# Optimization experiments

Measured on AMD Instinct MI355X. Metric: run time of the kernel, lower is better.

The kernel has to match this reference:

```python
import jax, jax.numpy as jnp
import numpy as np

# --- static configuration (mirrors init_kwargs) ---
L = 16        # latent_size
HL = 512      # hypernet_layer_size
D = 64        # decoder_layer_size
NDEC = 2      # decoder_n_layers
B, G = 128, 100  # batch, grid (pressure levels)
LOGP_MEAN, LOGP_STD = 0.0, 3.0
T_MEAN, T_STD = 1500.0, 500.0

# decoder layer structure generated by the hypernet
WEIGHT_SIZES = [(1, D)] + [(D, D)] * NDEC + [(D, 1)]
BIAS_SIZES = [1] + [D] * NDEC + [1]
OUT_SIZE = sum(a * b for a, b in WEIGHT_SIZES) + sum(BIAS_SIZES)  # 8450


def setup_inputs() -> dict:
    key = jax.random.key(0)
    ks = jax.random.split(key, 8)
    def init(k, shape, fan_in):
        return (jax.random.normal(k, shape, jnp.float32) / np.float32(np.sqrt(fan_in)))
    return {
        "z": jax.random.normal(ks[0], (B, L), jnp.float32),
        "log_P": jax.random.normal(ks[1], (B, G), jnp.float32) * 2.0,
        # hypernet MLP params: L -> HL -> HL -> HL -> OUT_SIZE
        "hW0": init(ks[2], (L, HL), L), "hb0": jnp.zeros((HL,), jnp.float32),
        "hW1": init(ks[3], (HL, HL), HL), "hb1": jnp.zeros((HL,), jnp.float32),
        "hW2": init(ks[4], (HL, HL), HL), "hb2": jnp.zeros((HL,), jnp.float32),
        "hWo": init(ks[5], (HL, OUT_SIZE), HL), "hbo": jnp.zeros((OUT_SIZE,), jnp.float32),
    }


def reference(z, log_P, hW0, hb0, hW1, hb1, hW2, hb2, hWo, hbo):
    Bsz, Gsz = log_P.shape
    R = Bsz * Gsz  # flattened rows
    # broadcast latent over the pressure grid: (B, L) -> (R, L)
    z_flat = jnp.broadcast_to(z[:, None, :], (Bsz, Gsz, z.shape[-1])).reshape(R, -1)
    # normalize pressure -> decoder input, shape (R, 1)
    x = (log_P.reshape(R, 1) - LOGP_MEAN) / LOGP_STD
    # hypernet MLP (leaky_relu, slope 0.01 like torch default)
    h = jax.nn.leaky_relu(z_flat @ hW0 + hb0)
    h = jax.nn.leaky_relu(h @ hW1 + hb1)
    h = jax.nn.leaky_relu(h @ hW2 + hb2)
    wab = h @ hWo + hbo  # (R, OUT_SIZE): per-row decoder weights+biases
    # per-row decoder: chain of batched GEMVs with siren activation
    off = 0
    n_layers = len(WEIGHT_SIZES)
    for i, ((di, do), bs) in enumerate(zip(WEIGHT_SIZES, BIAS_SIZES)):
        n = di * do
        w = wab[:, off:off + n].reshape(R, di, do)
        b = wab[:, off + n:off + n + bs]  # broadcasts against (R, do)
        off += n + bs
        x = jnp.einsum('bi,bij->bj', x, w) + b
        if i == 0:
            x = x * 30.0  # siren first-layer omega_0
        if i < n_layers - 1:
            x = jnp.sin(x)  # siren activation; last layer is Identity
    T_pred = x.reshape(Bsz, Gsz)
    # undo temperature normalization
    return T_pred * T_STD + T_MEAN
```

## Files before the change

### kernel.cpp

```cpp
#include <hip/hip_runtime.h>

#define WSTRIDE 8704

__device__ __forceinline__ float lrelu(float x) { return x > 0.0f ? x : 0.01f * x; }

__global__ __launch_bounds__(128) void h0T_kernel(const float* __restrict__ z,
                                                  const float* __restrict__ W,
                                                  const float* __restrict__ bias,
                                                  float* __restrict__ h0T) {
    int j = blockIdx.x;
    int b = threadIdx.x;
    float zr[16];
    *(float4*)&zr[0]  = *(const float4*)&z[b * 16 + 0];
    *(float4*)&zr[4]  = *(const float4*)&z[b * 16 + 4];
    *(float4*)&zr[8]  = *(const float4*)&z[b * 16 + 8];
    *(float4*)&zr[12] = *(const float4*)&z[b * 16 + 12];
    float acc = bias[j];
#pragma unroll
    for (int l = 0; l < 16; ++l) acc = fmaf(zr[l], W[l * 512 + j], acc);
    h0T[j * 128 + b] = lrelu(acc);
}

__global__ __launch_bounds__(512) void gemmT_kernel(const float* __restrict__ At,
                                                    const float* __restrict__ W,
                                                    const float* __restrict__ bias,
                                                    float* __restrict__ OT) {
    __shared__ __align__(16) float As[512][4];
    __shared__ float red[8][64][5];
    int jt = blockIdx.x & 7;
    int bt = blockIdx.x >> 3;
    int tid = threadIdx.x;
    int lane = tid & 63;
    int wid  = __builtin_amdgcn_readfirstlane(tid >> 6);
    int b0 = bt * 4;
#pragma unroll
    for (int r = 0; r < 2; ++r) {
        int p = r * 512 + tid;
        int k = p >> 1, q = p & 1;
        *(float2*)&As[k][q * 2] = *(const float2*)&At[k * 128 + b0 + q * 2];
    }
    __syncthreads();
    int j = jt * 64 + lane;
    float acc[4] = {};
    int k0 = wid * 64;
#pragma unroll 8
    for (int kk = 0; kk < 64; ++kk) {
        int k = k0 + kk;
        float4 a = *(const float4*)&As[k][0];
        float w = W[k * 512 + j];
        acc[0] = fmaf(a.x, w, acc[0]);
        acc[1] = fmaf(a.y, w, acc[1]);
        acc[2] = fmaf(a.z, w, acc[2]);
        acc[3] = fmaf(a.w, w, acc[3]);
    }
#pragma unroll
    for (int i = 0; i < 4; ++i) red[wid][lane][i] = acc[i];
    __syncthreads();
    if (tid < 256) {
        int jj = tid >> 2;
        int bb = tid & 3;
        float s = 0.f;
#pragma unroll
        for (int w = 0; w < 8; ++w) s += red[w][jj][bb];
        int jg = jt * 64 + jj;
        OT[jg * 128 + b0 + bb] = lrelu(s + bias[jg]);
    }
}

__global__ __launch_bounds__(256) void wabT_kernel(const float* __restrict__ At,
                                                   const float* __restrict__ W,
                                                   const float* __restrict__ bias,
                                                   float* __restrict__ wab) {
    __shared__ __align__(16) float smem[4352];
    float (*As)[8] = (float (*)[8])smem;
    int tid = threadIdx.x;
    int lane = tid & 63;
    int wid = __builtin_amdgcn_readfirstlane(tid >> 6);
    int jt = blockIdx.x >> 4;
    int bt = blockIdx.x & 15;
    if (jt >= 67) return;
    int b0 = bt * 8;
#pragma unroll
    for (int r = 0; r < 8; ++r) {
        int p = r * 256 + tid;
        int k = p >> 1, h = (p & 1) * 4;
        *(float4*)&As[k][h] = *(const float4*)&At[k * 128 + b0 + h];
    }
    __syncthreads();
    int j0r = jt * 128 + lane * 2;
    int j0 = j0r <= 8448 ? j0r : 8448;
    int k0 = wid * 128;
    const float* __restrict__ Wp = W + (size_t)k0 * 8450 + j0;
    float acc[8][2];
#pragma unroll
    for (int i = 0; i < 8; ++i) { acc[i][0] = 0.f; acc[i][1] = 0.f; }
#pragma unroll 4
    for (int kk = 0; kk < 128; ++kk) {
        float4 aL = *(const float4*)&As[k0 + kk][0];
        float4 aH = *(const float4*)&As[k0 + kk][4];
        float2 w = *(const float2*)(Wp + (size_t)kk * 8450);
        float av[8] = {aL.x, aL.y, aL.z, aL.w, aH.x, aH.y, aH.z, aH.w};
#pragma unroll
        for (int i = 0; i < 8; ++i) {
            acc[i][0] = fmaf(av[i], w.x, acc[i][0]);
            acc[i][1] = fmaf(av[i], w.y, acc[i][1]);
        }
    }
    __syncthreads();
#pragma unroll
    for (int i = 0; i < 8; ++i) {
        smem[(wid * 8 + i) * 132 + lane * 2 + 0] = acc[i][0];
        smem[(wid * 8 + i) * 132 + lane * 2 + 1] = acc[i][1];
    }
    __syncthreads();
    int j = tid & 127;
    int bs = tid >> 7;
    int jg = jt * 128 + j;
    if (jg < 8450) {
        float bj = bias[jg];
        int dst = jg + (jg >= 65 ? 3 : 0);
#pragma unroll
        for (int q = 0; q < 4; ++q) {
            int bb = bs * 4 + q;
            float s = smem[(0 * 8 + bb) * 132 + j] + smem[(1 * 8 + bb) * 132 + j]
                    + smem[(2 * 8 + bb) * 132 + j] + smem[(3 * 8 + bb) * 132 + j];
            wab[(size_t)(b0 + bb) * WSTRIDE + dst] = s + bj;
        }
    }
}

__global__ __launch_bounds__(512) void decoder_kernel(const float* __restrict__ wab,
                                                      const float* __restrict__ logP,
                                                      float* __restrict__ out) {
    __shared__ float hX[64 * 65];
    __shared__ float hY[64 * 65];
    __shared__ float red[8][68];
    int b  = blockIdx.x >> 1;
    int gh = blockIdx.x & 1;
    int tid = threadIdx.x;
    int lane = tid & 63;
    int jq = (tid >> 6) * 8;
    int g = gh * 64 + lane;
    bool act = g < 100;
    const float* __restrict__ row = wab + (size_t)b * WSTRIDE;
    float x0 = act ? logP[b * 100 + g] * (1.0f / 3.0f) : 0.0f;
    float c0 = row[64];
#pragma unroll
    for (int t = 0; t < 8; ++t)
        hX[(jq + t) * 65 + lane] = __sinf(30.0f * fmaf(x0, row[jq + t], c0));
    __syncthreads();
    {
        float a[8];
#pragma unroll
        for (int t = 0; t < 8; ++t) a[t] = row[4164 + jq + t];
#pragma unroll 4
        for (int i = 0; i < 64; ++i) {
            float hi = hX[i * 65 + lane];
            const float* wr = row + 68 + i * 64 + jq;
            float4 w0 = *(const float4*)&wr[0];
            float4 w1 = *(const float4*)&wr[4];
            a[0] = fmaf(hi, w0.x, a[0]);  a[1] = fmaf(hi, w0.y, a[1]);
            a[2] = fmaf(hi, w0.z, a[2]);  a[3] = fmaf(hi, w0.w, a[3]);
            a[4] = fmaf(hi, w1.x, a[4]);  a[5] = fmaf(hi, w1.y, a[5]);
            a[6] = fmaf(hi, w1.z, a[6]);  a[7] = fmaf(hi, w1.w, a[7]);
        }
#pragma unroll
        for (int t = 0; t < 8; ++t) hY[(jq + t) * 65 + lane] = __sinf(a[t]);
    }
    __syncthreads();
    {
        float a[8];
#pragma unroll
        for (int t = 0; t < 8; ++t) a[t] = row[8324 + jq + t];
#pragma unroll 4
        for (int i = 0; i < 64; ++i) {
            float hi = hY[i * 65 + lane];
            const float* wr = row + 4228 + i * 64 + jq;
            float4 w0 = *(const float4*)&wr[0];
            float4 w1 = *(const float4*)&wr[4];
            a[0] = fmaf(hi, w0.x, a[0]);  a[1] = fmaf(hi, w0.y, a[1]);
            a[2] = fmaf(hi, w0.z, a[2]);  a[3] = fmaf(hi, w0.w, a[3]);
            a[4] = fmaf(hi, w1.x, a[4]);  a[5] = fmaf(hi, w1.y, a[5]);
            a[6] = fmaf(hi, w1.z, a[6]);  a[7] = fmaf(hi, w1.w, a[7]);
        }
#pragma unroll
        for (int t = 0; t < 8; ++t) hX[(jq + t) * 65 + lane] = __sinf(a[t]);
    }
    __syncthreads();
    float p = 0.f;
#pragma unroll
    for (int t = 0; t < 8; ++t)
        p = fmaf(hX[(jq + t) * 65 + lane], row[8388 + jq + t], p);
    red[tid >> 6][lane] = p;
    __syncthreads();
    if (tid < 64 && act) {
        float s = row[8452];
#pragma unroll
        for (int w = 0; w < 8; ++w) s += red[w][lane];
        out[b * 100 + g] = fmaf(s, 500.0f, 1500.0f);
    }
}

extern "C" void kernel_launch(void* const* d_in, const int* in_sizes, int n_in,
                              void* d_out, int out_size, void* d_ws, size_t ws_size,
                              hipStream_t stream) {
    const float* z    = (const float*)d_in[0];
    const float* logP = (const float*)d_in[1];
    const float* hW0  = (const float*)d_in[2];
    const float* hb0  = (const float*)d_in[3];
    const float* hW1  = (const float*)d_in[4];
    const float* hb1  = (const float*)d_in[5];
    const float* hW2  = (const float*)d_in[6];
    const float* hb2  = (const float*)d_in[7];
    const float* hWo  = (const float*)d_in[8];
    const float* hbo  = (const float*)d_in[9];
    float* out = (float*)d_out;

    float* wab = (float*)d_ws;
    float* h0T = wab + 128 * WSTRIDE;
    float* h1T = h0T + 512 * 128;
    float* h2T = h1T + 512 * 128;

    h0T_kernel<<<512, 128, 0, stream>>>(z, hW0, hb0, h0T);
    gemmT_kernel<<<256, 512, 0, stream>>>(h0T, hW1, hb1, h1T);
    gemmT_kernel<<<256, 512, 0, stream>>>(h1T, hW2, hb2, h2T);
    wabT_kernel<<<1088, 256, 0, stream>>>(h2T, hWo, hbo, wab);
    decoder_kernel<<<256, 512, 0, stream>>>(wab, logP, out);
}
```

Baseline: 69.18 us.

## Fuse all five stages into one cooperative persistent kernel with grid syncs

```diff
diff --git a/kernel.cpp b/kernel.cpp
--- a/kernel.cpp
+++ b/kernel.cpp
@@ -1,35 +1,21 @@
 #include <hip/hip_runtime.h>
+#include <hip/hip_cooperative_groups.h>
+
+namespace cg = cooperative_groups;
 
 #define WSTRIDE 8704
 
 __device__ __forceinline__ float lrelu(float x) { return x > 0.0f ? x : 0.01f * x; }
 
-__global__ __launch_bounds__(128) void h0T_kernel(const float* __restrict__ z,
-                                                  const float* __restrict__ W,
-                                                  const float* __restrict__ bias,
-                                                  float* __restrict__ h0T) {
-    int j = blockIdx.x;
-    int b = threadIdx.x;
-    float zr[16];
-    *(float4*)&zr[0]  = *(const float4*)&z[b * 16 + 0];
-    *(float4*)&zr[4]  = *(const float4*)&z[b * 16 + 4];
-    *(float4*)&zr[8]  = *(const float4*)&z[b * 16 + 8];
-    *(float4*)&zr[12] = *(const float4*)&z[b * 16 + 12];
-    float acc = bias[j];
-#pragma unroll
-    for (int l = 0; l < 16; ++l) acc = fmaf(zr[l], W[l * 512 + j], acc);
-    h0T[j * 128 + b] = lrelu(acc);
-}
-
-__global__ __launch_bounds__(512) void gemmT_kernel(const float* __restrict__ At,
-                                                    const float* __restrict__ W,
-                                                    const float* __restrict__ bias,
-                                                    float* __restrict__ OT) {
-    __shared__ __align__(16) float As[512][4];
-    __shared__ float red[8][64][5];
+__device__ __forceinline__ void gemm512_phase(const float* __restrict__ At,
+                                              const float* __restrict__ W,
+                                              const float* __restrict__ bias,
+                                              float* __restrict__ Ot,
+                                              float* smem, int tid) {
+    float (*As)[4] = (float (*)[4])smem;
+    float (*red)[64][5] = (float (*)[64][5])(smem + 2048);
     int jt = blockIdx.x & 7;
     int bt = blockIdx.x >> 3;
-    int tid = threadIdx.x;
     int lane = tid & 63;
     int wid  = __builtin_amdgcn_readfirstlane(tid >> 6);
     int b0 = bt * 4;
@@ -63,141 +49,172 @@
 #pragma unroll
         for (int w = 0; w < 8; ++w) s += red[w][jj][bb];
         int jg = jt * 64 + jj;
-        OT[jg * 128 + b0 + bb] = lrelu(s + bias[jg]);
-    }
+        Ot[jg * 128 + b0 + bb] = lrelu(s + bias[jg]);
+    }
+    __syncthreads();
 }
 
-__global__ __launch_bounds__(256) void wabT_kernel(const float* __restrict__ At,
-                                                   const float* __restrict__ W,
-                                                   const float* __restrict__ bias,
-                                                   float* __restrict__ wab) {
-    __shared__ __align__(16) float smem[4352];
-    float (*As)[8] = (float (*)[8])smem;
+__global__ __launch_bounds__(512, 2)
+void fused_kernel(const float* __restrict__ z,    const float* __restrict__ logP,
+                  const float* __restrict__ hW0,  const float* __restrict__ hb0,
+                  const float* __restrict__ hW1,  const float* __restrict__ hb1,
+                  const float* __restrict__ hW2,  const float* __restrict__ hb2,
+                  const float* __restrict__ hWo,  const float* __restrict__ hbo,
+                  float* __restrict__ out,        float* __restrict__ wab,
+                  float* __restrict__ h0T,        float* __restrict__ h1T,
+                  float* __restrict__ h2T) {
+    __shared__ __align__(16) float smem[8960];
+    cg::grid_group grid = cg::this_grid();
     int tid = threadIdx.x;
-    int lane = tid & 63;
-    int wid = __builtin_amdgcn_readfirstlane(tid >> 6);
-    int jt = blockIdx.x >> 4;
-    int bt = blockIdx.x & 15;
-    if (jt >= 67) return;
-    int b0 = bt * 8;
-#pragma unroll
-    for (int r = 0; r < 8; ++r) {
-        int p = r * 256 + tid;
-        int k = p >> 1, h = (p & 1) * 4;
-        *(float4*)&As[k][h] = *(const float4*)&At[k * 128 + b0 + h];
-    }
-    __syncthreads();
-    int j0r = jt * 128 + lane * 2;
-    int j0 = j0r <= 8448 ? j0r : 8448;
-    int k0 = wid * 128;
-    const float* __restrict__ Wp = W + (size_t)k0 * 8450 + j0;
-    float acc[8][2];
-#pragma unroll
-    for (int i = 0; i < 8; ++i) { acc[i][0] = 0.f; acc[i][1] = 0.f; }
+
+    if (tid < 256) {
+        int j = blockIdx.x * 2 + (tid >> 7);
+        int b = tid & 127;
+        float zr[16];
+        *(float4*)&zr[0]  = *(const float4*)&z[b * 16 + 0];
+        *(float4*)&zr[4]  = *(const float4*)&z[b * 16 + 4];
+        *(float4*)&zr[8]  = *(const float4*)&z[b * 16 + 8];
+        *(float4*)&zr[12] = *(const float4*)&z[b * 16 + 12];
+        float acc = hb0[j];
+#pragma unroll
+        for (int l = 0; l < 16; ++l) acc = fmaf(zr[l], hW0[l * 512 + j], acc);
+        h0T[j * 128 + b] = lrelu(acc);
+    }
+    grid.sync();
+
+    gemm512_phase(h0T, hW1, hb1, h1T, smem, tid);
+    grid.sync();
+    gemm512_phase(h1T, hW2, hb2, h2T, smem, tid);
+    grid.sync();
+
+    {
+        float (*As)[8] = (float (*)[8])smem;
+        int lane = tid & 63;
+        int wid = __builtin_amdgcn_readfirstlane(tid >> 6);
+        for (int t = blockIdx.x; t < 1072; t += 256) {
+            int jt = t >> 4;
+            int bt = t & 15;
+            int b0 = bt * 8;
+#pragma unroll
+            for (int r = 0; r < 2; ++r) {
+                int p = r * 512 + tid;
+                int k = p >> 1, h = (p & 1) * 4;
+                *(float4*)&As[k][h] = *(const float4*)&h2T[k * 128 + b0 + h];
+            }
+            __syncthreads();
+            int j0r = jt * 128 + lane * 2;
+            int j0 = j0r <= 8448 ? j0r : 8448;
+            int k0 = wid * 64;
+            const float* __restrict__ Wp = hWo + (size_t)k0 * 8450 + j0;
+            float acc[8][2];
+#pragma unroll
+            for (int i = 0; i < 8; ++i) { acc[i][0] = 0.f; acc[i][1] = 0.f; }
 #pragma unroll 4
-    for (int kk = 0; kk < 128; ++kk) {
-        float4 aL = *(const float4*)&As[k0 + kk][0];
-        float4 aH = *(const float4*)&As[k0 + kk][4];
-        float2 w = *(const float2*)(Wp + (size_t)kk * 8450);
-        float av[8] = {aL.x, aL.y, aL.z, aL.w, aH.x, aH.y, aH.z, aH.w};
-#pragma unroll
-        for (int i = 0; i < 8; ++i) {
-            acc[i][0] = fmaf(av[i], w.x, acc[i][0]);
-            acc[i][1] = fmaf(av[i], w.y, acc[i][1]);
-        }
-    }
-    __syncthreads();
-#pragma unroll
-    for (int i = 0; i < 8; ++i) {
-        smem[(wid * 8 + i) * 132 + lane * 2 + 0] = acc[i][0];
-        smem[(wid * 8 + i) * 132 + lane * 2 + 1] = acc[i][1];
-    }
-    __syncthreads();
-    int j = tid & 127;
-    int bs = tid >> 7;
-    int jg = jt * 128 + j;
-    if (jg < 8450) {
-        float bj = bias[jg];
-        int dst = jg + (jg >= 65 ? 3 : 0);
-#pragma unroll
-        for (int q = 0; q < 4; ++q) {
-            int bb = bs * 4 + q;
-            float s = smem[(0 * 8 + bb) * 132 + j] + smem[(1 * 8 + bb) * 132 + j]
-                    + smem[(2 * 8 + bb) * 132 + j] + smem[(3 * 8 + bb) * 132 + j];
-            wab[(size_t)(b0 + bb) * WSTRIDE + dst] = s + bj;
-        }
-    }
-}
-
-__global__ __launch_bounds__(512) void decoder_kernel(const float* __restrict__ wab,
-                                                      const float* __restrict__ logP,
-                                                      float* __restrict__ out) {
-    __shared__ float hX[64 * 65];
-    __shared__ float hY[64 * 65];
-    __shared__ float red[8][68];
-    int b  = blockIdx.x >> 1;
-    int gh = blockIdx.x & 1;
-    int tid = threadIdx.x;
-    int lane = tid & 63;
-    int jq = (tid >> 6) * 8;
-    int g = gh * 64 + lane;
-    bool act = g < 100;
-    const float* __restrict__ row = wab + (size_t)b * WSTRIDE;
-    float x0 = act ? logP[b * 100 + g] * (1.0f / 3.0f) : 0.0f;
-    float c0 = row[64];
-#pragma unroll
-    for (int t = 0; t < 8; ++t)
-        hX[(jq + t) * 65 + lane] = __sinf(30.0f * fmaf(x0, row[jq + t], c0));
-    __syncthreads();
+            for (int kk = 0; kk < 64; ++kk) {
+                float4 aL = *(const float4*)&As[k0 + kk][0];
+                float4 aH = *(const float4*)&As[k0 + kk][4];
+                float2 w = *(const float2*)(Wp + (size_t)kk * 8450);
+                float av[8] = {aL.x, aL.y, aL.z, aL.w, aH.x, aH.y, aH.z, aH.w};
+#pragma unroll
+                for (int i = 0; i < 8; ++i) {
+                    acc[i][0] = fmaf(av[i], w.x, acc[i][0]);
+                    acc[i][1] = fmaf(av[i], w.y, acc[i][1]);
+                }
+            }
+            __syncthreads();
+#pragma unroll
+            for (int i = 0; i < 8; ++i) {
+                smem[(wid * 8 + i) * 132 + lane * 2 + 0] = acc[i][0];
+                smem[(wid * 8 + i) * 132 + lane * 2 + 1] = acc[i][1];
+            }
+            __syncthreads();
+            int j = tid & 127;
+            int bs = tid >> 7;
+            int jg = jt * 128 + j;
+            if (jg < 8450) {
+                float bj = hbo[jg];
+                int dst = jg + (jg >= 65 ? 3 : 0);
+#pragma unroll
+                for (int q = 0; q < 2; ++q) {
+                    int bb = bs * 2 + q;
+                    float s = 0.f;
+#pragma unroll
+                    for (int w = 0; w < 8; ++w) s += smem[(w * 8 + bb) * 132 + j];
+                    wab[(size_t)(b0 + bb) * WSTRIDE + dst] = s + bj;
+                }
+            }
+            __syncthreads();
+        }
+    }
+    grid.sync();
+
     {
-        float a[8];
-#pragma unroll
-        for (int t = 0; t < 8; ++t) a[t] = row[4164 + jq + t];
+        float* hX = smem;
+        float* hY = smem + 4160;
+        float* red = smem + 8320;
+        int b  = blockIdx.x >> 1;
+        int gh = blockIdx.x & 1;
+        int lane = tid & 63;
+        int jq = (tid >> 6) * 8;
+        int g = gh * 64 + lane;
+        bool act = g < 100;
+        const float* __restrict__ row = wab + (size_t)b * WSTRIDE;
+        float x0 = act ? logP[b * 100 + g] * (1.0f / 3.0f) : 0.0f;
+        float c0 = row[64];
+#pragma unroll
+        for (int t = 0; t < 8; ++t)
+            hX[(jq + t) * 65 + lane] = __sinf(30.0f * fmaf(x0, row[jq + t], c0));
+        __syncthreads();
+        {
+            float a[8];
+#pragma unroll
+            for (int t = 0; t < 8; ++t) a[t] = row[4164 + jq + t];
 #pragma unroll 4
-        for (int i = 0; i < 64; ++i) {
-            float hi = hX[i * 65 + lane];
-            const float* wr = row + 68 + i * 64 + jq;
-            float4 w0 = *(const float4*)&wr[0];
-            float4 w1 = *(const float4*)&wr[4];
-            a[0] = fmaf(hi, w0.x, a[0]);  a[1] = fmaf(hi, w0.y, a[1]);
-            a[2] = fmaf(hi, w0.z, a[2]);  a[3] = fmaf(hi, w0.w, a[3]);
-            a[4] = fmaf(hi, w1.x, a[4]);  a[5] = fmaf(hi, w1.y, a[5]);
-            a[6] = fmaf(hi, w1.z, a[6]);  a[7] = fmaf(hi, w1.w, a[7]);
-        }
-#pragma unroll
-        for (int t = 0; t < 8; ++t) hY[(jq + t) * 65 + lane] = __sinf(a[t]);
-    }
-    __syncthreads();
-    {
-        float a[8];
-#pragma unroll
-        for (int t = 0; t < 8; ++t) a[t] = row[8324 + jq + t];
+            for (int i = 0; i < 64; ++i) {
+                float hi = hX[i * 65 + lane];
+                const float* wr = row + 68 + i * 64 + jq;
+                float4 w0 = *(const float4*)&wr[0];
+                float4 w1 = *(const float4*)&wr[4];
+                a[0] = fmaf(hi, w0.x, a[0]);  a[1] = fmaf(hi, w0.y, a[1]);
+                a[2] = fmaf(hi, w0.z, a[2]);  a[3] = fmaf(hi, w0.w, a[3]);
+                a[4] = fmaf(hi, w1.x, a[4]);  a[5] = fmaf(hi, w1.y, a[5]);
+                a[6] = fmaf(hi, w1.z, a[6]);  a[7] = fmaf(hi, w1.w, a[7]);
+            }
+#pragma unroll
+            for (int t = 0; t < 8; ++t) hY[(jq + t) * 65 + lane] = __sinf(a[t]);
+        }
+        __syncthreads();
+        {
+            float a[8];
+#pragma unroll
+            for (int t = 0; t < 8; ++t) a[t] = row[8324 + jq + t];
 #pragma unroll 4
-        for (int i = 0; i < 64; ++i) {
-            float hi = hY[i * 65 + lane];
-            const float* wr = row + 4228 + i * 64 + jq;
-            float4 w0 = *(const float4*)&wr[0];
-            float4 w1 = *(const float4*)&wr[4];
-            a[0] = fmaf(hi, w0.x, a[0]);  a[1] = fmaf(hi, w0.y, a[1]);
-            a[2] = fmaf(hi, w0.z, a[2]);  a[3] = fmaf(hi, w0.w, a[3]);
-            a[4] = fmaf(hi, w1.x, a[4]);  a[5] = fmaf(hi, w1.y, a[5]);
-            a[6] = fmaf(hi, w1.z, a[6]);  a[7] = fmaf(hi, w1.w, a[7]);
-        }
-#pragma unroll
-        for (int t = 0; t < 8; ++t) hX[(jq + t) * 65 + lane] = __sinf(a[t]);
-    }
-    __syncthreads();
-    float p = 0.f;
-#pragma unroll
-    for (int t = 0; t < 8; ++t)
-        p = fmaf(hX[(jq + t) * 65 + lane], row[8388 + jq + t], p);
-    red[tid >> 6][lane] = p;
-    __syncthreads();
-    if (tid < 64 && act) {
-        float s = row[8452];
-#pragma unroll
-        for (int w = 0; w < 8; ++w) s += red[w][lane];
-        out[b * 100 + g] = fmaf(s, 500.0f, 1500.0f);
+            for (int i = 0; i < 64; ++i) {
+                float hi = hY[i * 65 + lane];
+                const float* wr = row + 4228 + i * 64 + jq;
+                float4 w0 = *(const float4*)&wr[0];
+                float4 w1 = *(const float4*)&wr[4];
+                a[0] = fmaf(hi, w0.x, a[0]);  a[1] = fmaf(hi, w0.y, a[1]);
+                a[2] = fmaf(hi, w0.z, a[2]);  a[3] = fmaf(hi, w0.w, a[3]);
+                a[4] = fmaf(hi, w1.x, a[4]);  a[5] = fmaf(hi, w1.y, a[5]);
+                a[6] = fmaf(hi, w1.z, a[6]);  a[7] = fmaf(hi, w1.w, a[7]);
+            }
+#pragma unroll
+            for (int t = 0; t < 8; ++t) hX[(jq + t) * 65 + lane] = __sinf(a[t]);
+        }
+        __syncthreads();
+        float p = 0.f;
+#pragma unroll
+        for (int t = 0; t < 8; ++t)
+            p = fmaf(hX[(jq + t) * 65 + lane], row[8388 + jq + t], p);
+        red[(tid >> 6) * 68 + lane] = p;
+        __syncthreads();
+        if (tid < 64 && act) {
+            float s = row[8452];
+#pragma unroll
+            for (int w = 0; w < 8; ++w) s += red[w * 68 + lane];
+            out[b * 100 + g] = fmaf(s, 500.0f, 1500.0f);
+        }
     }
 }
 
@@ -221,9 +238,8 @@
     float* h1T = h0T + 512 * 128;
     float* h2T = h1T + 512 * 128;
 
-    h0T_kernel<<<512, 128, 0, stream>>>(z, hW0, hb0, h0T);
-    gemmT_kernel<<<256, 512, 0, stream>>>(h0T, hW1, hb1, h1T);
-    gemmT_kernel<<<256, 512, 0, stream>>>(h1T, hW2, hb2, h2T);
-    wabT_kernel<<<1088, 256, 0, stream>>>(h2T, hWo, hbo, wab);
-    decoder_kernel<<<256, 512, 0, stream>>>(wab, logP, out);
+    void* args[] = {&z, &logP, &hW0, &hb0, &hW1, &hb1, &hW2, &hb2,
+                    &hWo, &hbo, &out, &wab, &h0T, &h1T, &h2T};
+    hipLaunchCooperativeKernel((void*)fused_kernel, dim3(256), dim3(512),
+                               args, 0, stream);
 }
```

New measurement: 189.1 us. 173% more time.

## Retile hypernet GEMMs with register blocking and drop shared-memory A staging

Applied to the files above, without the earlier changes.

```diff
diff --git a/kernel.cpp b/kernel.cpp
--- a/kernel.cpp
+++ b/kernel.cpp
@@ -25,106 +25,126 @@
                                                     const float* __restrict__ W,
                                                     const float* __restrict__ bias,
                                                     float* __restrict__ OT) {
-    __shared__ __align__(16) float As[512][4];
     __shared__ float red[8][64][5];
     int jt = blockIdx.x & 7;
     int bt = blockIdx.x >> 3;
     int tid = threadIdx.x;
     int lane = tid & 63;
     int wid  = __builtin_amdgcn_readfirstlane(tid >> 6);
-    int b0 = bt * 4;
-#pragma unroll
-    for (int r = 0; r < 2; ++r) {
-        int p = r * 512 + tid;
-        int k = p >> 1, q = p & 1;
-        *(float2*)&As[k][q * 2] = *(const float2*)&At[k * 128 + b0 + q * 2];
-    }
-    __syncthreads();
-    int j = jt * 64 + lane;
+    int jg = lane & 15;
+    int bg = lane >> 4;
+    int j0 = jt * 64 + jg * 4;
+    int b  = bt * 4 + bg;
+    int k0 = wid * 64;
     float acc[4] = {};
-    int k0 = wid * 64;
-#pragma unroll 8
+#pragma unroll 4
     for (int kk = 0; kk < 64; ++kk) {
         int k = k0 + kk;
-        float4 a = *(const float4*)&As[k][0];
-        float w = W[k * 512 + j];
-        acc[0] = fmaf(a.x, w, acc[0]);
-        acc[1] = fmaf(a.y, w, acc[1]);
-        acc[2] = fmaf(a.z, w, acc[2]);
-        acc[3] = fmaf(a.w, w, acc[3]);
-    }
-#pragma unroll
-    for (int i = 0; i < 4; ++i) red[wid][lane][i] = acc[i];
+        float a = At[k * 128 + b];
+        float4 wv = *(const float4*)&W[k * 512 + j0];
+        acc[0] = fmaf(a, wv.x, acc[0]);
+        acc[1] = fmaf(a, wv.y, acc[1]);
+        acc[2] = fmaf(a, wv.z, acc[2]);
+        acc[3] = fmaf(a, wv.w, acc[3]);
+    }
+#pragma unroll
+    for (int e = 0; e < 4; ++e) red[wid][lane][e] = acc[e];
     __syncthreads();
     if (tid < 256) {
+        int bl = tid & 3;
         int jj = tid >> 2;
-        int bb = tid & 3;
+        int lane_r = bl * 16 + (jj >> 2);
+        int e_r = jj & 3;
         float s = 0.f;
 #pragma unroll
-        for (int w = 0; w < 8; ++w) s += red[w][jj][bb];
-        int jg = jt * 64 + jj;
-        OT[jg * 128 + b0 + bb] = lrelu(s + bias[jg]);
-    }
-}
-
-__global__ __launch_bounds__(256) void wabT_kernel(const float* __restrict__ At,
-                                                   const float* __restrict__ W,
-                                                   const float* __restrict__ bias,
-                                                   float* __restrict__ wab) {
-    __shared__ __align__(16) float smem[4352];
-    float (*As)[8] = (float (*)[8])smem;
+        for (int w = 0; w < 8; ++w) s += red[w][lane_r][e_r];
+        int jglob = jt * 64 + jj;
+        OT[jglob * 128 + bt * 4 + bl] = lrelu(s + bias[jglob]);
+    }
+}
+
+__global__ __launch_bounds__(256, 2) void wabT_kernel(const float* __restrict__ At,
+                                                      const float* __restrict__ W,
+                                                      const float* __restrict__ bias,
+                                                      float* __restrict__ wab) {
+    __shared__ float red[4 * 64 * 32];
     int tid = threadIdx.x;
     int lane = tid & 63;
     int wid = __builtin_amdgcn_readfirstlane(tid >> 6);
-    int jt = blockIdx.x >> 4;
-    int bt = blockIdx.x & 15;
-    if (jt >= 67) return;
-    int b0 = bt * 8;
-#pragma unroll
-    for (int r = 0; r < 8; ++r) {
-        int p = r * 256 + tid;
-        int k = p >> 1, h = (p & 1) * 4;
-        *(float4*)&As[k][h] = *(const float4*)&At[k * 128 + b0 + h];
-    }
-    __syncthreads();
-    int j0r = jt * 128 + lane * 2;
-    int j0 = j0r <= 8448 ? j0r : 8448;
+    int B = blockIdx.x;
+    int idx = (B & 7) * 64 + (B >> 3);
+    int jt = idx >> 3;
+    int bt = idx & 7;
+    int jg = lane & 15;
+    int bg = lane >> 4;
+    int j0 = jt * 128 + jg * 8;
+    int b0 = bt * 16 + bg * 4;
     int k0 = wid * 128;
+    const float* __restrict__ Ap = At + k0 * 128 + b0;
     const float* __restrict__ Wp = W + (size_t)k0 * 8450 + j0;
-    float acc[8][2];
-#pragma unroll
-    for (int i = 0; i < 8; ++i) { acc[i][0] = 0.f; acc[i][1] = 0.f; }
+    float acc[4][8];
+#pragma unroll
+    for (int i = 0; i < 4; ++i)
+#pragma unroll
+        for (int jj = 0; jj < 8; ++jj) acc[i][jj] = 0.f;
 #pragma unroll 4
     for (int kk = 0; kk < 128; ++kk) {
-        float4 aL = *(const float4*)&As[k0 + kk][0];
-        float4 aH = *(const float4*)&As[k0 + kk][4];
-        float2 w = *(const float2*)(Wp + (size_t)kk * 8450);
-        float av[8] = {aL.x, aL.y, aL.z, aL.w, aH.x, aH.y, aH.z, aH.w};
-#pragma unroll
-        for (int i = 0; i < 8; ++i) {
-            acc[i][0] = fmaf(av[i], w.x, acc[i][0]);
-            acc[i][1] = fmaf(av[i], w.y, acc[i][1]);
-        }
-    }
-    __syncthreads();
-#pragma unroll
-    for (int i = 0; i < 8; ++i) {
-        smem[(wid * 8 + i) * 132 + lane * 2 + 0] = acc[i][0];
-        smem[(wid * 8 + i) * 132 + lane * 2 + 1] = acc[i][1];
-    }
-    __syncthreads();
-    int j = tid & 127;
-    int bs = tid >> 7;
-    int jg = jt * 128 + j;
-    if (jg < 8450) {
-        float bj = bias[jg];
-        int dst = jg + (jg >= 65 ? 3 : 0);
-#pragma unroll
-        for (int q = 0; q < 4; ++q) {
-            int bb = bs * 4 + q;
-            float s = smem[(0 * 8 + bb) * 132 + j] + smem[(1 * 8 + bb) * 132 + j]
-                    + smem[(2 * 8 + bb) * 132 + j] + smem[(3 * 8 + bb) * 132 + j];
-            wab[(size_t)(b0 + bb) * WSTRIDE + dst] = s + bj;
+        float4 a = *(const float4*)(Ap + kk * 128);
+        const float* wr = Wp + (size_t)kk * 8450;
+        float2 u0 = *(const float2*)(wr + 0);
+        float2 u1 = *(const float2*)(wr + 2);
+        float2 u2 = *(const float2*)(wr + 4);
+        float2 u3 = *(const float2*)(wr + 6);
+        float av[4] = {a.x, a.y, a.z, a.w};
+        float wv[8] = {u0.x, u0.y, u1.x, u1.y, u2.x, u2.y, u3.x, u3.y};
+#pragma unroll
+        for (int i = 0; i < 4; ++i)
+#pragma unroll
+            for (int jj = 0; jj < 8; ++jj)
+                acc[i][jj] = fmaf(av[i], wv[jj], acc[i][jj]);
+    }
+#pragma unroll
+    for (int i = 0; i < 4; ++i)
+#pragma unroll
+        for (int jj = 0; jj < 8; ++jj) {
+            int e = i * 8 + jj;
+            red[wid * 2048 + lane * 32 + (e ^ (lane & 31))] = acc[i][jj];
+        }
+    __syncthreads();
+    {
+        int bl = tid >> 4;
+        int jgr = tid & 15;
+        int lane_r = (bl >> 2) * 16 + jgr;
+        int swz = lane_r & 31;
+        float* drow = wab + (size_t)(bt * 16 + bl) * WSTRIDE;
+#pragma unroll
+        for (int r = 0; r < 8; ++r) {
+            int e = (bl & 3) * 8 + r;
+            int o = lane_r * 32 + (e ^ swz);
+            float s = red[o] + red[2048 + o] + red[4096 + o] + red[6144 + o];
+            int jglob = jt * 128 + jgr * 8 + r;
+            drow[jglob + (jglob >= 65 ? 3 : 0)] = s + bias[jglob];
+        }
+    }
+    {
+        int slot = tid >> 4;
+        int u = slot * 512 + B;
+        if (u < 4128) {
+            int c = 8192 + (u >> 4);
+            int oct = u & 15;
+            int sub = tid & 15;
+            int b = oct * 8 + (sub & 7);
+            int kh = sub >> 3;
+            float at = 0.f;
+            int kbase = kh * 256;
+#pragma unroll 8
+            for (int k = 0; k < 256; ++k) {
+                int kg = kbase + k;
+                at = fmaf(At[kg * 128 + b], W[(size_t)kg * 8450 + c], at);
+            }
+            float other = __shfl_xor(at, 8);
+            if (sub < 8)
+                wab[(size_t)b * WSTRIDE + c + 3] = at + other + bias[c];
         }
     }
 }
@@ -224,6 +244,6 @@
     h0T_kernel<<<512, 128, 0, stream>>>(z, hW0, hb0, h0T);
     gemmT_kernel<<<256, 512, 0, stream>>>(h0T, hW1, hb1, h1T);
     gemmT_kernel<<<256, 512, 0, stream>>>(h1T, hW2, hb2, h2T);
-    wabT_kernel<<<1088, 256, 0, stream>>>(h2T, hWo, hbo, wab);
+    wabT_kernel<<<512, 256, 0, stream>>>(h2T, hWo, hbo, wab);
     decoder_kernel<<<256, 512, 0, stream>>>(wab, logP, out);
 }
```

Result: slower. 83.75 us (+21.1%).

## Retile wab GEMM per-thread into 2 batches by 8 columns and swizzle block order

Applied to the files above, without the earlier changes.

```diff
diff --git a/kernel.cpp b/kernel.cpp
--- a/kernel.cpp
+++ b/kernel.cpp
@@ -67,64 +67,79 @@
     }
 }
 
-__global__ __launch_bounds__(256) void wabT_kernel(const float* __restrict__ At,
-                                                   const float* __restrict__ W,
-                                                   const float* __restrict__ bias,
-                                                   float* __restrict__ wab) {
-    __shared__ __align__(16) float smem[4352];
+__global__ __launch_bounds__(256, 4) void wabT_kernel(const float* __restrict__ At,
+                                                      const float* __restrict__ W,
+                                                      const float* __restrict__ bias,
+                                                      float* __restrict__ wab) {
+    __shared__ __align__(16) float smem[4 * 64 * 17];
     float (*As)[8] = (float (*)[8])smem;
     int tid = threadIdx.x;
     int lane = tid & 63;
     int wid = __builtin_amdgcn_readfirstlane(tid >> 6);
-    int jt = blockIdx.x >> 4;
-    int bt = blockIdx.x & 15;
+    int wgid = (blockIdx.x & 7) * 136 + (blockIdx.x >> 3);
+    int jt = wgid >> 4;
+    int bt = wgid & 15;
     if (jt >= 67) return;
-    int b0 = bt * 8;
-#pragma unroll
-    for (int r = 0; r < 8; ++r) {
+    int b0blk = bt * 8;
+#pragma unroll
+    for (int r = 0; r < 4; ++r) {
         int p = r * 256 + tid;
         int k = p >> 1, h = (p & 1) * 4;
-        *(float4*)&As[k][h] = *(const float4*)&At[k * 128 + b0 + h];
-    }
-    __syncthreads();
-    int j0r = jt * 128 + lane * 2;
-    int j0 = j0r <= 8448 ? j0r : 8448;
+        *(float4*)&As[k][h] = *(const float4*)&At[k * 128 + b0blk + h];
+    }
+    __syncthreads();
+    int jg = lane & 15;
+    int bg = lane >> 4;
+    int j0r = jt * 128 + jg * 8;
+    int j0 = j0r <= 8442 ? j0r : 8442;
     int k0 = wid * 128;
     const float* __restrict__ Wp = W + (size_t)k0 * 8450 + j0;
-    float acc[8][2];
-#pragma unroll
-    for (int i = 0; i < 8; ++i) { acc[i][0] = 0.f; acc[i][1] = 0.f; }
+    float acc[2][8];
+#pragma unroll
+    for (int i = 0; i < 2; ++i)
+#pragma unroll
+        for (int jj = 0; jj < 8; ++jj) acc[i][jj] = 0.f;
 #pragma unroll 4
     for (int kk = 0; kk < 128; ++kk) {
-        float4 aL = *(const float4*)&As[k0 + kk][0];
-        float4 aH = *(const float4*)&As[k0 + kk][4];
-        float2 w = *(const float2*)(Wp + (size_t)kk * 8450);
-        float av[8] = {aL.x, aL.y, aL.z, aL.w, aH.x, aH.y, aH.z, aH.w};
-#pragma unroll
-        for (int i = 0; i < 8; ++i) {
-            acc[i][0] = fmaf(av[i], w.x, acc[i][0]);
-            acc[i][1] = fmaf(av[i], w.y, acc[i][1]);
-        }
-    }
-    __syncthreads();
-#pragma unroll
-    for (int i = 0; i < 8; ++i) {
-        smem[(wid * 8 + i) * 132 + lane * 2 + 0] = acc[i][0];
-        smem[(wid * 8 + i) * 132 + lane * 2 + 1] = acc[i][1];
-    }
-    __syncthreads();
-    int j = tid & 127;
-    int bs = tid >> 7;
-    int jg = jt * 128 + j;
-    if (jg < 8450) {
-        float bj = bias[jg];
-        int dst = jg + (jg >= 65 ? 3 : 0);
+        float2 a = *(const float2*)&As[k0 + kk][bg * 2];
+        const float* wr = Wp + (size_t)kk * 8450;
+        float2 u0 = *(const float2*)(wr + 0);
+        float2 u1 = *(const float2*)(wr + 2);
+        float2 u2 = *(const float2*)(wr + 4);
+        float2 u3 = *(const float2*)(wr + 6);
+        float wv[8] = {u0.x, u0.y, u1.x, u1.y, u2.x, u2.y, u3.x, u3.y};
+#pragma unroll
+        for (int jj = 0; jj < 8; ++jj) {
+            acc[0][jj] = fmaf(a.x, wv[jj], acc[0][jj]);
+            acc[1][jj] = fmaf(a.y, wv[jj], acc[1][jj]);
+        }
+    }
+    __syncthreads();
+#pragma unroll
+    for (int bbi = 0; bbi < 2; ++bbi)
+#pragma unroll
+        for (int jj = 0; jj < 8; ++jj)
+            smem[(wid * 64 + lane) * 17 + bbi * 8 + jj] = acc[bbi][jj];
+    __syncthreads();
+    {
+        int j = tid & 127;
+        int bs = tid >> 7;
+        int jgr = j >> 3;
+        int jli = j & 7;
+        int jgl = jt * 128 + jgr * 8;
+        int jbase = jgl <= 8442 ? jgl : 8442;
+        int jglob = jbase + jli;
+        float bj = bias[jglob];
+        int dst = jglob + (jglob >= 65 ? 3 : 0);
 #pragma unroll
         for (int q = 0; q < 4; ++q) {
-            int bb = bs * 4 + q;
-            float s = smem[(0 * 8 + bb) * 132 + j] + smem[(1 * 8 + bb) * 132 + j]
-                    + smem[(2 * 8 + bb) * 132 + j] + smem[(3 * 8 + bb) * 132 + j];
-            wab[(size_t)(b0 + bb) * WSTRIDE + dst] = s + bj;
+            int bl = bs * 4 + q;
+            int lane_r = (bl >> 1) * 16 + jgr;
+            int i = (bl & 1) * 8 + jli;
+            float s = 0.f;
+#pragma unroll
+            for (int w = 0; w < 4; ++w) s += smem[(w * 64 + lane_r) * 17 + i];
+            wab[(size_t)(b0blk + bl) * WSTRIDE + dst] = s + bj;
         }
     }
 }
```

Measured after the change: 78.68 us. 1.14x slower.
